# Performance work log

Measured on AMD Instinct MI355X. Metric: run time of the kernel, lower is better.

The kernel has to match this reference:

```python
import jax, jax.numpy as jnp
import numpy as np
from jax import lax

STRIDE = 4

def crelu(x, b):
    # cReLU: x * (x >= bias)
    return x * (x >= b).astype(x.dtype)

def rbf_conv(x, w, stride):
    # Distance-based conv: per output pixel, dist[b,o] = sum_c ||window[b,c]-w[o,c]||_2,
    # std = std(dist over (B,O)) per pixel (torch.std, ddof=1), out = exp(-dist^2/(2 std^2)).
    B, C, H, W = x.shape
    O, Cw, kh, kw = w.shape
    Hp = (H - kh) // stride + 1
    Wp = (W - kw) // stride + 1
    # patches: [B, C*kh*kw, Hp, Wp], channel-major feature order
    patches = lax.conv_general_dilated_patches(x, (kh, kw), (stride, stride), 'VALID')
    patches = patches.reshape(B, C, kh * kw, Hp * Wp)
    wf = w.reshape(O, Cw, kh * kw)
    if Cw == 1 and C > 1:
        # RBF_Conv2d reuses the same single-channel weight for every input channel
        wf = jnp.broadcast_to(wf, (O, C, kh * kw))
    pn = (patches ** 2).sum(2)                       # [B,C,P]
    wn = (wf ** 2).sum(2)                            # [O,C]
    dot = jnp.einsum('bcfp,ocf->bocp', patches, wf)  # [B,O,C,P]
    d2 = jnp.maximum(pn[:, None] + wn[None, :, :, None] - 2.0 * dot, 1e-12)
    dist = jnp.sqrt(d2).sum(2)                       # [B,O,P] sum of per-channel L2 dists
    m = dist.mean((0, 1), keepdims=True)
    var = ((dist - m) ** 2).sum((0, 1), keepdims=True) / (B * O - 1)
    std = jnp.sqrt(var)                              # per-pixel std, ddof=1
    out = jnp.exp(-(dist ** 2) / (2.0 * std ** 2))   # gaussian RBF
    return out.reshape(B, O, Hp, Wp)

def sfm(x, shape, filt, kernel, alpha0=0.9):
    # SFM temporal filtering: weight response map by alpha^seq pattern, pool by filter, re-tile
    seg_h, seg_w = shape
    C = x.shape[1]
    rm = x.transpose(0, 2, 3, 1).reshape(-1, seg_h, seg_w, C)   # get_RM
    seq = jnp.arange(filt[0] * filt[1], dtype=x.dtype)[::-1]
    alpha = (jnp.asarray(alpha0, x.dtype) ** seq).reshape(filt)
    alpha = jnp.tile(alpha, (seg_h // filt[0], seg_w // filt[1]))[None, :, :, None]
    out = (rm * alpha).reshape(-1, seg_h // filt[0], filt[0], seg_w // filt[1], filt[1], C)
    out = out.mean(axis=(2, 4))
    return out.reshape(-1, 1, kernel[0], kernel[1])

def setup_inputs():
    key = jax.random.key(0)
    ks = jax.random.split(key, 8)
    def kaiming(k, shape):
        fan_in = int(np.prod(shape[1:]))
        bound = 1.0 / np.sqrt(fan_in)
        w = jax.random.uniform(k, shape, jnp.float32, -bound, bound)
        return w.at[0].set(0.0)  # reset_parameters zeroes filter 0
    x = jax.random.uniform(ks[0], (4096, 3, 28, 28), jnp.float32)
    rgb_w = kaiming(ks[1], (100, 3, 5, 5))
    w2 = kaiming(ks[2], (225, 1, 10, 10))
    w3 = kaiming(ks[3], (625, 1, 15, 15))
    w4 = kaiming(ks[4], (1225, 1, 25, 25))
    fcb = 1.0 / np.sqrt(1225.0)
    fc_w = jax.random.uniform(ks[5], (10, 1225), jnp.float32, -fcb, fcb)
    fc_b = jax.random.uniform(ks[6], (10,), jnp.float32, -fcb, fcb)
    return {"x": x, "rgb_w": rgb_w, "w2": w2, "w3": w3, "w4": w4, "fc_w": fc_w, "fc_b": fc_b}

def reference(x, rgb_w, w2, w3, w4, fc_w, fc_b):
    B = x.shape[0]
    out = crelu(rbf_conv(x, rgb_w, STRIDE), 0.4)   # RGB_preprocess -> [B,100,6,6]
    out = sfm(out, (6, 6), (2, 2), (10, 10))       # layer1 SFM -> [B*9,1,10,10]
    out = crelu(rbf_conv(out, w2, STRIDE), 0.1)    # -> [B*9,225,1,1]
    out = sfm(out, (3, 3), (1, 3), (15, 15))       # -> [B*3,1,15,15]
    out = crelu(rbf_conv(out, w3, STRIDE), 0.01)   # -> [B*3,625,1,1]
    out = sfm(out, (3, 1), (3, 1), (25, 25))       # -> [B,1,25,25]
    out = crelu(rbf_conv(out, w4, STRIDE), 0.01)   # -> [B,1225,1,1]
    return out.reshape(B, -1) @ fc_w.T + fc_b      # fc1 -> [B,10]
```

## Files before the change

### kernel.cpp

```cpp
#include <hip/hip_runtime.h>
#include <hip/hip_bf16.h>
#include <math.h>

#define DIV_UP(a,b) (((a)+(b)-1)/(b))
#define FSQRT(x) __builtin_amdgcn_sqrtf(x)

typedef __attribute__((ext_vector_type(8))) short short8;
typedef __attribute__((ext_vector_type(4))) float f32x4;

#define GL16(g, l) __builtin_amdgcn_global_load_lds( \
    (const __attribute__((address_space(1))) void*)(g), \
    (__attribute__((address_space(3))) void*)(l), 16, 0, 0)

#define SCALE_FROM_PART(OUTVAR) \
    __shared__ double ss_[256], qq_[256]; \
    __shared__ float ssc_; \
    { int t_ = threadIdx.x; double s_ = 0.0, q_ = 0.0; \
      for (int i_ = t_; i_ < nb; i_ += 256) { s_ += part[2*i_]; q_ += part[2*i_+1]; } \
      ss_[t_] = s_; qq_[t_] = q_; __syncthreads(); \
      for (int st_ = 128; st_ > 0; st_ >>= 1) { \
          if (t_ < st_) { ss_[t_] += ss_[t_+st_]; qq_[t_] += qq_[t_+st_]; } \
          __syncthreads(); } \
      if (t_ == 0) { double m_ = ss_[0] / Nstat; \
          double var_ = (qq_[0] - Nstat*m_*m_) / (Nstat - 1.0); \
          ssc_ = (float)(0.5 / var_); } \
      __syncthreads(); } \
    float OUTVAR = ssc_;

__device__ __forceinline__ void splitnorm_row(
    const float* __restrict__ src, ushort* __restrict__ H, ushort* __restrict__ L,
    float* __restrict__ norm, int R, int K, int Kp, int row, int lane) {
    float s = 0.f;
    if (row < R) {
        for (int k = lane; k < Kp; k += 64) {
            float v = (k < K) ? src[(size_t)row*K + k] : 0.f;
            __hip_bfloat16 hb = __float2bfloat16(v);
            float hf = __bfloat162float(hb);
            __hip_bfloat16 lb = __float2bfloat16(v - hf);
            H[(size_t)row*Kp + k] = *(ushort*)&hb;
            L[(size_t)row*Kp + k] = *(ushort*)&lb;
            float r = hf + __bfloat162float(lb);
            s += r*r;
        }
    } else {
        for (int k = lane; k < Kp; k += 64) {
            H[(size_t)row*Kp + k] = 0;
            L[(size_t)row*Kp + k] = 0;
        }
    }
    for (int off = 32; off > 0; off >>= 1) s += __shfl_down(s, off, 64);
    if (lane == 0) norm[row] = s;
}

__global__ __launch_bounds__(256) void prep_all_kernel(
    const float* __restrict__ w1, ushort* __restrict__ W1h, ushort* __restrict__ W1l,
    float* __restrict__ wn1,
    const float* __restrict__ w2, ushort* __restrict__ W2h, ushort* __restrict__ W2l,
    float* __restrict__ wn2,
    const float* __restrict__ w3, ushort* __restrict__ W3h, ushort* __restrict__ W3l,
    float* __restrict__ wn3,
    const float* __restrict__ w4, ushort* __restrict__ W4h, ushort* __restrict__ W4l,
    float* __restrict__ wn4,
    int frontload) {
    int blk = blockIdx.x;
    int wave = threadIdx.x >> 6, lane = threadIdx.x & 63;
    if (blk < 84) {
        int j = blk*4 + wave;
        if (j >= 336) return;
        int o = j / 3, c = j - o*3;
        float s = 0.f;
        if (lane < 32) {
            int k = lane;
            float v = (o < 100 && k < 25) ? w1[o*75 + c*25 + k] : 0.f;
            __hip_bfloat16 hb = __float2bfloat16(v);
            float hf = __bfloat162float(hb);
            __hip_bfloat16 lb = __float2bfloat16(v - hf);
            W1h[o*96 + c*32 + k] = *(ushort*)&hb;
            W1l[o*96 + c*32 + k] = *(ushort*)&lb;
            float r = hf + __bfloat162float(lb);
            s = r*r;
        }
#pragma unroll
        for (int off = 16; off > 0; off >>= 1) s += __shfl_down(s, off, 64);
        if (lane == 0) wn1[j] = s;
    } else if (!frontload) {
        return;
    } else if (blk < 148) {
        int row = (blk - 84)*4 + wave;
        splitnorm_row(w2, W2h, W2l, wn2, 225, 100, 128, row, lane);
    } else if (blk < 308) {
        int row = (blk - 148)*4 + wave;
        splitnorm_row(w3, W3h, W3l, wn3, 625, 225, 256, row, lane);
    } else {
        int row = (blk - 308)*4 + wave;
        splitnorm_row(w4, W4h, W4l, wn4, 1225, 625, 640, row, lane);
    }
}

__global__ __launch_bounds__(256) void splitnorm_kernel(
    const float* __restrict__ src, ushort* __restrict__ H, ushort* __restrict__ L,
    float* __restrict__ norm, int R, int K, int Kp) {
    int wave = threadIdx.x >> 6, lane = threadIdx.x & 63;
    int row = blockIdx.x*4 + wave;
    splitnorm_row(src, H, L, norm, R, K, Kp, row, lane);
}

__global__ __launch_bounds__(512, 2) void rbf1_mfma(
    const float* __restrict__ x, const ushort* __restrict__ Wh, const ushort* __restrict__ Wl,
    const float* __restrict__ wn1, float* __restrict__ dist1,
    float* __restrict__ pixstat) {
    __shared__ ushort Ah[3*144*32];
    __shared__ ushort Al[3*144*32];
    __shared__ float pnl[432];
    __shared__ float rstat[7*144*2];
    int tid = threadIdx.x;
    int b4 = blockIdx.x;

    if (tid < 432) {
        int row = tid / 3, c = tid - row*3;
        int img = row / 36, p = row - img*36;
        int ph = p / 6, pw = p - ph*6;
        const float* xp = x + (size_t)b4*9408 + img*2352 + c*784 + (ph*28 + pw)*4;
        float arr[25];
#pragma unroll
        for (int ki = 0; ki < 5; ++ki) {
            float4 v4 = *(const float4*)(xp + ki*28);
            arr[ki*5+0] = v4.x; arr[ki*5+1] = v4.y;
            arr[ki*5+2] = v4.z; arr[ki*5+3] = v4.w;
            arr[ki*5+4] = xp[ki*28 + 4];
        }
        float pnc = 0.f;
        int tilebase = c*9216 + row*64;
        int r3 = (row >> 1) & 3;
#pragma unroll
        for (int kb = 0; kb < 4; ++kb) {
            uint4 hq, lq;
            uint* hqa = (uint*)&hq;
            uint* lqa = (uint*)&lq;
#pragma unroll
            for (int j = 0; j < 4; ++j) {
                int k0 = kb*8 + 2*j;
                float v0 = (k0 < 25) ? arr[k0] : 0.f;
                float v1 = (k0+1 < 25) ? arr[k0+1] : 0.f;
                __hip_bfloat16 h0 = __float2bfloat16(v0);
                float hf0 = __bfloat162float(h0);
                __hip_bfloat16 l0 = __float2bfloat16(v0 - hf0);
                float r0 = hf0 + __bfloat162float(l0);
                __hip_bfloat16 h1 = __float2bfloat16(v1);
                float hf1 = __bfloat162float(h1);
                __hip_bfloat16 l1 = __float2bfloat16(v1 - hf1);
                float r1 = hf1 + __bfloat162float(l1);
                pnc += r0*r0 + r1*r1;
                hqa[j] = (uint)(*(ushort*)&h0) | ((uint)(*(ushort*)&h1) << 16);
                lqa[j] = (uint)(*(ushort*)&l0) | ((uint)(*(ushort*)&l1) << 16);
            }
            int kbs = kb ^ r3;
            *(uint4*)((char*)Ah + tilebase + kbs*16) = hq;
            *(uint4*)((char*)Al + tilebase + kbs*16) = lq;
        }
        pnl[tid] = pnc;
    }
    __syncthreads();

    int lane = tid & 63, wave = tid >> 6;
    if (wave < 7) {
        int nf = wave;
        int rl = lane & 15, kh = lane >> 4;
        int o = nf*16 + rl;
        const ushort* bhp = Wh + o*96 + kh*8;
        const ushort* blp = Wl + o*96 + kh*8;
        short8 bh0 = *(const short8*)(bhp);
        short8 bh1 = *(const short8*)(bhp + 32);
        short8 bh2 = *(const short8*)(bhp + 64);
        short8 bl0 = *(const short8*)(blp);
        short8 bl1 = *(const short8*)(blp + 32);
        short8 bl2 = *(const short8*)(blp + 64);
        float w0 = wn1[o*3], w1v = wn1[o*3+1], w2v = wn1[o*3+2];
        int swz = (rl >> 1) & 3;
        int kx = (kh ^ swz) * 16;
        bool valid = (o < 100);
        float* mystat = rstat + wave*288;
#pragma unroll
        for (int mf = 0; mf < 9; ++mf) {
            int rbase = (mf*16 + rl)*64;
            short8 ah0 = *(const short8*)((const char*)Ah + rbase + kx);
            short8 al0 = *(const short8*)((const char*)Al + rbase + kx);
            short8 ah1 = *(const short8*)((const char*)Ah + 9216 + rbase + kx);
            short8 al1 = *(const short8*)((const char*)Al + 9216 + rbase + kx);
            short8 ah2 = *(const short8*)((const char*)Ah + 18432 + rbase + kx);
            short8 al2 = *(const short8*)((const char*)Al + 18432 + rbase + kx);
            f32x4 a0 = {0.f,0.f,0.f,0.f}, a1 = {0.f,0.f,0.f,0.f}, a2 = {0.f,0.f,0.f,0.f};
            a0 = __builtin_amdgcn_mfma_f32_16x16x32_bf16(ah0, bh0, a0, 0, 0, 0);
            a1 = __builtin_amdgcn_mfma_f32_16x16x32_bf16(ah1, bh1, a1, 0, 0, 0);
            a2 = __builtin_amdgcn_mfma_f32_16x16x32_bf16(ah2, bh2, a2, 0, 0, 0);
            a0 = __builtin_amdgcn_mfma_f32_16x16x32_bf16(ah0, bl0, a0, 0, 0, 0);
            a1 = __builtin_amdgcn_mfma_f32_16x16x32_bf16(ah1, bl1, a1, 0, 0, 0);
            a2 = __builtin_amdgcn_mfma_f32_16x16x32_bf16(ah2, bl2, a2, 0, 0, 0);
            a0 = __builtin_amdgcn_mfma_f32_16x16x32_bf16(al0, bh0, a0, 0, 0, 0);
            a1 = __builtin_amdgcn_mfma_f32_16x16x32_bf16(al1, bh1, a1, 0, 0, 0);
            a2 = __builtin_amdgcn_mfma_f32_16x16x32_bf16(al2, bh2, a2, 0, 0, 0);
            float dsum[4], dsq[4];
            size_t base = (size_t)(b4*144 + mf*16 + kh*4)*100 + o;
#pragma unroll
            for (int r = 0; r < 4; ++r) {
                int row = mf*16 + kh*4 + r;
                float d = FSQRT(fmaxf(pnl[row*3+0] + w0  - 2.f*a0[r], 1e-12f))
                        + FSQRT(fmaxf(pnl[row*3+1] + w1v - 2.f*a1[r], 1e-12f))
                        + FSQRT(fmaxf(pnl[row*3+2] + w2v - 2.f*a2[r], 1e-12f));
                float dv = valid ? d : 0.f;
                if (valid) dist1[base + (size_t)r*100] = d;
                dsum[r] = dv; dsq[r] = dv*dv;
            }
#pragma unroll
            for (int m = 1; m <= 8; m <<= 1) {
#pragma unroll
                for (int r = 0; r < 4; ++r) {
                    dsum[r] += __shfl_xor(dsum[r], m, 64);
                    dsq[r]  += __shfl_xor(dsq[r],  m, 64);
                }
            }
            if (rl == 0) {
#pragma unroll
                for (int r = 0; r < 4; ++r) {
                    int row = mf*16 + kh*4 + r;
                    mystat[row*2]     = dsum[r];
                    mystat[row*2 + 1] = dsq[r];
                }
            }
        }
    }
    __syncthreads();
    if (tid < 72) {
        int p = tid >> 1, w = tid & 1;
        float s = 0.f;
#pragma unroll
        for (int wv = 0; wv < 7; ++wv)
#pragma unroll
            for (int g = 0; g < 4; ++g)
                s += rstat[wv*288 + (p + 36*g)*2 + w];
        pixstat[(size_t)b4*72 + 2*p + w] = s;
    }
}

__global__ __launch_bounds__(256) void finalize36_kernel(
    const float* __restrict__ pixstat, float* __restrict__ scale) {
    __shared__ double ss[256], qq[256];
    int p = blockIdx.x, tid = threadIdx.x;
    double s = 0.0, q = 0.0;
    for (int b = tid; b < 1024; b += 256) {
        s += (double)pixstat[(size_t)b*72 + 2*p];
        q += (double)pixstat[(size_t)b*72 + 2*p + 1];
    }
    ss[tid] = s; qq[tid] = q; __syncthreads();
    for (int st = 128; st > 0; st >>= 1) {
        if (tid < st) { ss[tid] += ss[tid+st]; qq[tid] += qq[tid+st]; }
        __syncthreads();
    }
    if (tid == 0) {
        const double N = 409600.0;
        double m = ss[0] / N;
        double var = (qq[0] - N*m*m) / (N - 1.0);
        scale[p] = (float)(0.5 / var);
    }
}

__global__ __launch_bounds__(256) void sfm1_kernel(
    const float* __restrict__ dist1, const float* __restrict__ scale,
    float* __restrict__ y2) {
    int gid = blockIdx.x*256 + threadIdx.x;
    if (gid >= 36864*100) return;
    int c = gid % 100, n = gid / 100;
    int b = n / 9, ij = n % 9, i = ij / 3, j = ij % 3;
    const float alpha[2][2] = {{0.729f, 0.81f},{0.9f, 1.0f}};
    float acc = 0.f;
#pragma unroll
    for (int fh = 0; fh < 2; ++fh)
#pragma unroll
        for (int fw = 0; fw < 2; ++fw) {
            int p = (2*i+fh)*6 + (2*j+fw);
            float d = dist1[(size_t)b*3600 + p*100 + c];
            float v = __expf(-d*d*scale[p]);
            v = (v >= 0.4f) ? v : 0.f;
            acc += alpha[fh][fw]*v;
        }
    y2[gid] = 0.25f * acc;
}

__global__ __launch_bounds__(256) void sfm1s_kernel(
    const float* __restrict__ dist1, const float* __restrict__ scale,
    ushort* __restrict__ H, ushort* __restrict__ L, float* __restrict__ norm) {
    int wave = threadIdx.x >> 6, lane = threadIdx.x & 63;
    int n = blockIdx.x*4 + wave;
    int b = n / 9, ij = n % 9, i = ij / 3, j = ij % 3;
    const float alpha[2][2] = {{0.729f, 0.81f},{0.9f, 1.0f}};
    float s = 0.f;
#pragma unroll
    for (int q = 0; q < 2; ++q) {
        int k = lane + q*64;
        float y = 0.f;
        if (k < 100) {
            float acc = 0.f;
#pragma unroll
            for (int fh = 0; fh < 2; ++fh)
#pragma unroll
                for (int fw = 0; fw < 2; ++fw) {
                    int p = (2*i+fh)*6 + (2*j+fw);
                    float d = dist1[(size_t)b*3600 + p*100 + k];
                    float v = __expf(-d*d*scale[p]);
                    v = (v >= 0.4f) ? v : 0.f;
                    acc += alpha[fh][fw]*v;
                }
            y = 0.25f * acc;
        }
        __hip_bfloat16 hb = __float2bfloat16(y);
        float hf = __bfloat162float(hb);
        __hip_bfloat16 lb = __float2bfloat16(y - hf);
        H[(size_t)n*128 + k] = *(ushort*)&hb;
        L[(size_t)n*128 + k] = *(ushort*)&lb;
        float r = hf + __bfloat162float(lb);
        s += r*r;
    }
    for (int off = 32; off > 0; off >>= 1) s += __shfl_down(s, off, 64);
    if (lane == 0) norm[n] = s;
}

__global__ __launch_bounds__(256) void sfm2s_kernel(
    const float* __restrict__ dist2, const double* __restrict__ part, int nb, double Nstat,
    ushort* __restrict__ H, ushort* __restrict__ L, float* __restrict__ norm) {
    SCALE_FROM_PART(s2);
    int wave = threadIdx.x >> 6, lane = threadIdx.x & 63;
    int n2 = blockIdx.x*4 + wave;
    int b = n2 / 3, i = n2 % 3;
    const float alphaJ[3] = {0.81f, 0.9f, 1.0f};
    float s = 0.f;
#pragma unroll
    for (int q = 0; q < 4; ++q) {
        int k = lane + q*64;
        float y = 0.f;
        if (k < 225) {
            float acc = 0.f;
#pragma unroll
            for (int j = 0; j < 3; ++j) {
                float d = dist2[((size_t)(b*9 + i*3 + j))*225 + k];
                float v = __expf(-d*d*s2);
                v = (v >= 0.1f) ? v : 0.f;
                acc += alphaJ[j]*v;
            }
            y = acc * (1.f/3.f);
        }
        __hip_bfloat16 hb = __float2bfloat16(y);
        float hf = __bfloat162float(hb);
        __hip_bfloat16 lb = __float2bfloat16(y - hf);
        H[(size_t)n2*256 + k] = *(ushort*)&hb;
        L[(size_t)n2*256 + k] = *(ushort*)&lb;
        float r = hf + __bfloat162float(lb);
        s += r*r;
    }
    for (int off = 32; off > 0; off >>= 1) s += __shfl_down(s, off, 64);
    if (lane == 0) norm[n2] = s;
}

__global__ __launch_bounds__(256) void sfm3s_kernel(
    const float* __restrict__ dist3, const double* __restrict__ part, int nb, double Nstat,
    ushort* __restrict__ H, ushort* __restrict__ L, float* __restrict__ norm) {
    SCALE_FROM_PART(s3);
    int wave = threadIdx.x >> 6, lane = threadIdx.x & 63;
    int b = blockIdx.x*4 + wave;
    const float alphaI[3] = {0.81f, 0.9f, 1.0f};
    float s = 0.f;
#pragma unroll
    for (int q = 0; q < 10; ++q) {
        int k = lane + q*64;
        float y = 0.f;
        if (k < 625) {
            float acc = 0.f;
#pragma unroll
            for (int i = 0; i < 3; ++i) {
                float d = dist3[((size_t)(b*3 + i))*625 + k];
                float v = __expf(-d*d*s3);
                v = (v >= 0.01f) ? v : 0.f;
                acc += alphaI[i]*v;
            }
            y = acc * (1.f/3.f);
        }
        __hip_bfloat16 hb = __float2bfloat16(y);
        float hf = __bfloat162float(hb);
        __hip_bfloat16 lb = __float2bfloat16(y - hf);
        H[(size_t)b*640 + k] = *(ushort*)&hb;
        L[(size_t)b*640 + k] = *(ushort*)&lb;
        float r = hf + __bfloat162float(lb);
        s += r*r;
    }
    for (int off = 32; off > 0; off >>= 1) s += __shfl_down(s, off, 64);
    if (lane == 0) norm[b] = s;
}

__global__ __launch_bounds__(512, 4) void distg_mfma(
    const ushort* __restrict__ Yh, const ushort* __restrict__ Yl,
    const ushort* __restrict__ Wh, const ushort* __restrict__ Wl,
    const float* __restrict__ pn, const float* __restrict__ wn,
    float* __restrict__ D, int N, int O, int Kp,
    double* __restrict__ part) {
    __shared__ ushort Ahs[2048], Als[2048], Bhs[4096], Bls[4096];
    __shared__ double wred[8][2];
    int tid = threadIdx.x, lane = tid & 63, wave = tid >> 6;
    int bn = blockIdx.x * 64, bo = blockIdx.y * 128;
    int wm = wave >> 2, wq = wave & 3;

    int rL = lane >> 2, cL = lane & 3;
    int cs = cL ^ ((rL >> 1) & 3);
    size_t boff = (size_t)(bo + wave*16 + rL) * Kp + cs*8;
    ushort* lBh = Bhs + wave*512;
    ushort* lBl = Bls + wave*512;
    int aw = wave & 3;
    size_t aoff = (size_t)(bn + aw*16 + rL) * Kp + cs*8;
    ushort* lA = ((wave < 4) ? Ahs : Als) + aw*512;
    const ushort* Asrc = (wave < 4) ? Yh : Yl;

    int rl = lane & 15, kh = lane >> 4;
    int kbs_r = kh ^ ((rl >> 1) & 3);
    int raoff[2], rboff[2];
#pragma unroll
    for (int mf = 0; mf < 2; ++mf) raoff[mf] = (wm*32 + mf*16 + rl)*64 + kbs_r*16;
#pragma unroll
    for (int nf = 0; nf < 2; ++nf) rboff[nf] = (wq*32 + nf*16 + rl)*64 + kbs_r*16;

    f32x4 acc[2][2];
#pragma unroll
    for (int mf = 0; mf < 2; ++mf)
#pragma unroll
        for (int nf = 0; nf < 2; ++nf) acc[mf][nf] = (f32x4){0.f,0.f,0.f,0.f};

    int NT = Kp >> 5;
    for (int t = 0; t < NT; ++t) {
        int k0 = t*32;
        GL16(Asrc + aoff + k0, lA);
        GL16(Wh + boff + k0, lBh);
        GL16(Wl + boff + k0, lBl);
        __syncthreads();
        short8 a_h[2], a_l[2];
#pragma unroll
        for (int mf = 0; mf < 2; ++mf) {
            a_h[mf] = *(const short8*)((const char*)Ahs + raoff[mf]);
            a_l[mf] = *(const short8*)((const char*)Als + raoff[mf]);
        }
#pragma unroll
        for (int nf = 0; nf < 2; ++nf) {
            short8 b_h = *(const short8*)((const char*)Bhs + rboff[nf]);
            short8 b_l = *(const short8*)((const char*)Bls + rboff[nf]);
#pragma unroll
            for (int mf = 0; mf < 2; ++mf) {
                acc[mf][nf] = __builtin_amdgcn_mfma_f32_16x16x32_bf16(a_h[mf], b_h, acc[mf][nf], 0, 0, 0);
                acc[mf][nf] = __builtin_amdgcn_mfma_f32_16x16x32_bf16(a_h[mf], b_l, acc[mf][nf], 0, 0, 0);
                acc[mf][nf] = __builtin_amdgcn_mfma_f32_16x16x32_bf16(a_l[mf], b_h, acc[mf][nf], 0, 0, 0);
            }
        }
        __syncthreads();
    }

    double lsum = 0.0, lsq = 0.0;
#pragma unroll
    for (int mf = 0; mf < 2; ++mf) {
#pragma unroll
        for (int r = 0; r < 4; ++r) {
            int n = bn + wm*32 + mf*16 + kh*4 + r;
            float pv = pn[n];
#pragma unroll
            for (int nf = 0; nf < 2; ++nf) {
                int o = bo + wq*32 + nf*16 + rl;
                if (o < O) {
                    float d2 = pv + wn[o] - 2.f*acc[mf][nf][r];
                    float dd = FSQRT(fmaxf(d2, 1e-12f));
                    D[(size_t)n*O + o] = dd;
                    lsum += dd; lsq += (double)dd*dd;
                }
            }
        }
    }
    for (int off = 32; off > 0; off >>= 1) {
        lsum += __shfl_down(lsum, off, 64);
        lsq  += __shfl_down(lsq,  off, 64);
    }
    if (lane == 0) { wred[wave][0] = lsum; wred[wave][1] = lsq; }
    __syncthreads();
    if (tid == 0) {
        double s = 0.0, q = 0.0;
#pragma unroll
        for (int w = 0; w < 8; ++w) { s += wred[w][0]; q += wred[w][1]; }
        int bid = blockIdx.y * gridDim.x + blockIdx.x;
        part[2*bid]   = s;
        part[2*bid+1] = q;
    }
}

__global__ __launch_bounds__(256) void fc_kernel(
    const float* __restrict__ dist4, const double* __restrict__ part, int nb, double Nstat,
    const float* __restrict__ fcw, const float* __restrict__ fcb,
    float* __restrict__ out) {
    SCALE_FROM_PART(s4);
    int b = blockIdx.x;
    int tid = threadIdx.x;
    float acc[10] = {};
    for (int o = tid; o < 1225; o += 256) {
        float d = dist4[(size_t)b*1225 + o];
        float v = __expf(-d*d*s4);
        v = (v >= 0.01f) ? v : 0.f;
#pragma unroll
        for (int k = 0; k < 10; ++k) acc[k] += v * fcw[k*1225 + o];
    }
    __shared__ float red[10*256];
#pragma unroll
    for (int k = 0; k < 10; ++k) red[k*256 + tid] = acc[k];
    __syncthreads();
    for (int st = 128; st > 0; st >>= 1) {
        if (tid < st) {
#pragma unroll
            for (int k = 0; k < 10; ++k) red[k*256 + tid] += red[k*256 + tid + st];
        }
        __syncthreads();
    }
    if (tid < 10) out[b*10 + tid] = red[tid*256] + fcb[tid];
}

extern "C" void kernel_launch(void* const* d_in, const int* in_sizes, int n_in,
                              void* d_out, int out_size, void* d_ws, size_t ws_size,
                              hipStream_t stream) {
    const float* x     = (const float*)d_in[0];
    const float* rgb_w = (const float*)d_in[1];
    const float* w2    = (const float*)d_in[2];
    const float* w3    = (const float*)d_in[3];
    const float* w4    = (const float*)d_in[4];
    const float* fc_w  = (const float*)d_in[5];
    const float* fc_b  = (const float*)d_in[6];
    float* out = (float*)d_out;

    float* wsf   = (float*)d_ws;
    float* dist  = wsf;
    float* ybuf  = wsf + 14745600;
    float* pnb   = ybuf + 3686400;
    float* wnb2  = pnb + 36864;
    float* wnb3  = wnb2 + 256;
    float* wnb4  = wnb3 + 640;
    float* scale = wnb4 + 1280;
    double* pblk = (double*)(scale + 64);
    float* wsend = (float*)(pblk + 2304);

    ushort* W1h = (ushort*)pnb;
    ushort* W1l = W1h + 10752;
    float*  wn1 = (float*)(W1l + 10752);

    float* pixstat = ybuf;

    size_t base_floats = (size_t)(wsend - wsf);
    size_t y2_floats   = 2u * 36864u * 128u / 2u;
    size_t w2_floats   = 2u * 256u * 128u / 2u;
    bool roomy = ws_size >= (base_floats + y2_floats + w2_floats + 1024) * sizeof(float);

    ushort* Y2h = roomy ? (ushort*)wsend : (ushort*)(dist + 8388608);
    ushort* Y2l = Y2h + 36864*128;
    ushort* W2h = roomy ? (Y2l + 36864*128) : ((ushort*)(dist + 8388608) + 2*36864*128);
    ushort* W2l = W2h + 256*128;
    ushort* Y3h = (ushort*)ybuf;
    ushort* Y3l = Y3h + 12288*256;
    ushort* Y4h = (ushort*)ybuf;
    ushort* Y4l = Y4h + 4096*640;
    ushort* W4h = Y4l + 4096*640;
    ushort* W4l = W4h + 1280*640;
    ushort* W3h = roomy ? (ushort*)(ybuf + 3522560) : (Y3l + 12288*256);
    ushort* W3l = W3h + 640*256;

    prep_all_kernel<<<628, 256, 0, stream>>>(
        rgb_w, W1h, W1l, wn1,
        w2, W2h, W2l, wnb2,
        w3, W3h, W3l, wnb3,
        w4, W4h, W4l, wnb4,
        roomy ? 1 : 0);

    rbf1_mfma<<<1024, 512, 0, stream>>>(x, W1h, W1l, wn1, dist, pixstat);
    finalize36_kernel<<<36, 256, 0, stream>>>(pixstat, scale);

    if (roomy) {
        sfm1s_kernel<<<36864/4, 256, 0, stream>>>(dist, scale, Y2h, Y2l, pnb);
    } else {
        sfm1_kernel<<<DIV_UP(36864*100,256), 256, 0, stream>>>(dist, scale, ybuf);
        splitnorm_kernel<<<36864/4, 256, 0, stream>>>(ybuf, Y2h, Y2l, pnb, 36864, 100, 128);
        splitnorm_kernel<<<256/4, 256, 0, stream>>>(w2, W2h, W2l, wnb2, 225, 100, 128);
    }

    distg_mfma<<<dim3(576,2), 512, 0, stream>>>(Y2h, Y2l, W2h, W2l, pnb, wnb2, dist, 36864, 225, 128, pblk);
    sfm2s_kernel<<<12288/4, 256, 0, stream>>>(dist, pblk, 1152, 8294400.0, Y3h, Y3l, pnb);

    if (!roomy) splitnorm_kernel<<<640/4, 256, 0, stream>>>(w3, W3h, W3l, wnb3, 625, 225, 256);
    distg_mfma<<<dim3(192,5), 512, 0, stream>>>(Y3h, Y3l, W3h, W3l, pnb, wnb3, dist, 12288, 625, 256, pblk);
    sfm3s_kernel<<<4096/4, 256, 0, stream>>>(dist, pblk, 960, 7680000.0, Y4h, Y4l, pnb);

    if (!roomy) splitnorm_kernel<<<1280/4, 256, 0, stream>>>(w4, W4h, W4l, wnb4, 1225, 625, 640);
    distg_mfma<<<dim3(64,10), 512, 0, stream>>>(Y4h, Y4l, W4h, W4l, pnb, wnb4, dist, 4096, 1225, 640, pblk);

    fc_kernel<<<4096, 256, 0, stream>>>(dist, pblk, 640, 5017600.0, fc_w, fc_b, out);
}
```

Baseline: 191.4 us.

## Fold weight prep into rbf1 kernel and build layer-1 B fragments in registers

Removes the separate prep kernel launch. Each rbf1 wave now converts its layer-1 weights to bf16 hi/lo fragments and computes their norms directly in registers, reading the fp32 weights from global memory. The w2/w3/w4 split-norm preparation is carried by 272 extra blocks appended to the rbf1 grid. This saves one launch and a global round trip for W1, but every rbf1 block now redoes the weight conversion, and the extra prep blocks compete with the main work.

```diff
diff --git a/kernel.cpp b/kernel.cpp
--- a/kernel.cpp
+++ b/kernel.cpp
@@ -27,6 +27,22 @@
       __syncthreads(); } \
     float OUTVAR = ssc_;
 
+#define BUILD_B(C, BH, BL, WN) { \
+    float s_ = 0.f; short8 hv_, lv_; \
+    _Pragma("unroll") \
+    for (int j_ = 0; j_ < 8; ++j_) { \
+        int k_ = kh*8 + j_; \
+        float v_ = (valid && k_ < 25) ? w1g[o*75 + (C)*25 + k_] : 0.f; \
+        __hip_bfloat16 hb_ = __float2bfloat16(v_); \
+        float hf_ = __bfloat162float(hb_); \
+        __hip_bfloat16 lb_ = __float2bfloat16(v_ - hf_); \
+        hv_[j_] = *(short*)&hb_; lv_[j_] = *(short*)&lb_; \
+        float r_ = hf_ + __bfloat162float(lb_); \
+        s_ += r_*r_; } \
+    s_ += __shfl_xor(s_, 16, 64); \
+    s_ += __shfl_xor(s_, 32, 64); \
+    BH = hv_; BL = lv_; WN = s_; }
+
 __device__ __forceinline__ void splitnorm_row(
     const float* __restrict__ src, ushort* __restrict__ H, ushort* __restrict__ L,
     float* __restrict__ norm, int R, int K, int Kp, int row, int lane) {
@@ -52,51 +68,6 @@
     if (lane == 0) norm[row] = s;
 }
 
-__global__ __launch_bounds__(256) void prep_all_kernel(
-    const float* __restrict__ w1, ushort* __restrict__ W1h, ushort* __restrict__ W1l,
-    float* __restrict__ wn1,
-    const float* __restrict__ w2, ushort* __restrict__ W2h, ushort* __restrict__ W2l,
-    float* __restrict__ wn2,
-    const float* __restrict__ w3, ushort* __restrict__ W3h, ushort* __restrict__ W3l,
-    float* __restrict__ wn3,
-    const float* __restrict__ w4, ushort* __restrict__ W4h, ushort* __restrict__ W4l,
-    float* __restrict__ wn4,
-    int frontload) {
-    int blk = blockIdx.x;
-    int wave = threadIdx.x >> 6, lane = threadIdx.x & 63;
-    if (blk < 84) {
-        int j = blk*4 + wave;
-        if (j >= 336) return;
-        int o = j / 3, c = j - o*3;
-        float s = 0.f;
-        if (lane < 32) {
-            int k = lane;
-            float v = (o < 100 && k < 25) ? w1[o*75 + c*25 + k] : 0.f;
-            __hip_bfloat16 hb = __float2bfloat16(v);
-            float hf = __bfloat162float(hb);
-            __hip_bfloat16 lb = __float2bfloat16(v - hf);
-            W1h[o*96 + c*32 + k] = *(ushort*)&hb;
-            W1l[o*96 + c*32 + k] = *(ushort*)&lb;
-            float r = hf + __bfloat162float(lb);
-            s = r*r;
-        }
-#pragma unroll
-        for (int off = 16; off > 0; off >>= 1) s += __shfl_down(s, off, 64);
-        if (lane == 0) wn1[j] = s;
-    } else if (!frontload) {
-        return;
-    } else if (blk < 148) {
-        int row = (blk - 84)*4 + wave;
-        splitnorm_row(w2, W2h, W2l, wn2, 225, 100, 128, row, lane);
-    } else if (blk < 308) {
-        int row = (blk - 148)*4 + wave;
-        splitnorm_row(w3, W3h, W3l, wn3, 625, 225, 256, row, lane);
-    } else {
-        int row = (blk - 308)*4 + wave;
-        splitnorm_row(w4, W4h, W4l, wn4, 1225, 625, 640, row, lane);
-    }
-}
-
 __global__ __launch_bounds__(256) void splitnorm_kernel(
     const float* __restrict__ src, ushort* __restrict__ H, ushort* __restrict__ L,
     float* __restrict__ norm, int R, int K, int Kp) {
@@ -106,14 +77,25 @@
 }
 
 __global__ __launch_bounds__(512, 2) void rbf1_mfma(
-    const float* __restrict__ x, const ushort* __restrict__ Wh, const ushort* __restrict__ Wl,
-    const float* __restrict__ wn1, float* __restrict__ dist1,
-    float* __restrict__ pixstat) {
+    const float* __restrict__ x, const float* __restrict__ w1g,
+    float* __restrict__ dist1, float* __restrict__ pixstat,
+    const float* __restrict__ w2, ushort* __restrict__ W2h, ushort* __restrict__ W2l, float* __restrict__ wn2,
+    const float* __restrict__ w3, ushort* __restrict__ W3h, ushort* __restrict__ W3l, float* __restrict__ wn3,
+    const float* __restrict__ w4, ushort* __restrict__ W4h, ushort* __restrict__ W4l, float* __restrict__ wn4) {
     __shared__ ushort Ah[3*144*32];
     __shared__ ushort Al[3*144*32];
     __shared__ float pnl[432];
     __shared__ float rstat[7*144*2];
     int tid = threadIdx.x;
+
+    if (blockIdx.x >= 1024) {
+        int wv = tid >> 6, ln = tid & 63;
+        int prow = (blockIdx.x - 1024)*8 + wv;
+        if (prow < 256)      splitnorm_row(w2, W2h, W2l, wn2, 225, 100, 128, prow, ln);
+        else if (prow < 896) splitnorm_row(w3, W3h, W3l, wn3, 625, 225, 256, prow-256, ln);
+        else                 splitnorm_row(w4, W4h, W4l, wn4, 1225, 625, 640, prow-896, ln);
+        return;
+    }
     int b4 = blockIdx.x;
 
     if (tid < 432) {
@@ -167,18 +149,14 @@
         int nf = wave;
         int rl = lane & 15, kh = lane >> 4;
         int o = nf*16 + rl;
-        const ushort* bhp = Wh + o*96 + kh*8;
-        const ushort* blp = Wl + o*96 + kh*8;
-        short8 bh0 = *(const short8*)(bhp);
-        short8 bh1 = *(const short8*)(bhp + 32);
-        short8 bh2 = *(const short8*)(bhp + 64);
-        short8 bl0 = *(const short8*)(blp);
-        short8 bl1 = *(const short8*)(blp + 32);
-        short8 bl2 = *(const short8*)(blp + 64);
-        float w0 = wn1[o*3], w1v = wn1[o*3+1], w2v = wn1[o*3+2];
+        bool valid = (o < 100);
+        short8 bh0, bh1, bh2, bl0, bl1, bl2;
+        float w0, w1v, w2v;
+        BUILD_B(0, bh0, bl0, w0);
+        BUILD_B(1, bh1, bl1, w1v);
+        BUILD_B(2, bh2, bl2, w2v);
         int swz = (rl >> 1) & 3;
         int kx = (kh ^ swz) * 16;
-        bool valid = (o < 100);
         float* mystat = rstat + wave*288;
 #pragma unroll
         for (int mf = 0; mf < 9; ++mf) {
@@ -545,10 +523,6 @@
     double* pblk = (double*)(scale + 64);
     float* wsend = (float*)(pblk + 2304);
 
-    ushort* W1h = (ushort*)pnb;
-    ushort* W1l = W1h + 10752;
-    float*  wn1 = (float*)(W1l + 10752);
-
     float* pixstat = ybuf;
 
     size_t base_floats = (size_t)(wsend - wsf);
@@ -569,14 +543,11 @@
     ushort* W3h = roomy ? (ushort*)(ybuf + 3522560) : (Y3l + 12288*256);
     ushort* W3l = W3h + 640*256;
 
-    prep_all_kernel<<<628, 256, 0, stream>>>(
-        rgb_w, W1h, W1l, wn1,
+    rbf1_mfma<<<roomy ? 1296 : 1024, 512, 0, stream>>>(
+        x, rgb_w, dist, pixstat,
         w2, W2h, W2l, wnb2,
         w3, W3h, W3l, wnb3,
-        w4, W4h, W4l, wnb4,
-        roomy ? 1 : 0);
-
-    rbf1_mfma<<<1024, 512, 0, stream>>>(x, W1h, W1l, wn1, dist, pixstat);
+        w4, W4h, W4l, wnb4);
     finalize36_kernel<<<36, 256, 0, stream>>>(pixstat, scale);
 
     if (roomy) {
```

After: 187.4 us. -2.1%, faster.
